# Optimization experiments

Measured on AMD Instinct MI355X. Metric: run time of the kernel, lower is better.

## Reference

```python
import jax, jax.numpy as jnp
import numpy as np

NU, NI, NR = 50000, 50000, 5   # users, items, rating levels
D, B, LS, LI = 64, 512, 32, 64 # embed_dim, batch, max social nbrs, max item hist
NEG = -1e9


def setup_inputs() -> dict:
    key = jax.random.key(0)
    ks = iter(jax.random.split(key, 64))
    def lin(din, dout):
        s = 1.0 / np.sqrt(din)
        return (jax.random.uniform(next(ks), (din, dout), minval=-s, maxval=s, dtype=jnp.float32),
                jax.random.uniform(next(ks), (dout,), minval=-s, maxval=s, dtype=jnp.float32))
    inp = {}
    inp['user_w'] = jax.random.normal(next(ks), (NU, D), dtype=jnp.float32) * 0.1
    inp['item_w'] = jax.random.normal(next(ks), (NI, D), dtype=jnp.float32) * 0.1
    inp['rating_w'] = jax.random.normal(next(ks), (NR, D), dtype=jnp.float32) * 0.1
    for name, din, dout in [('i_ln1', 2*D, D), ('i_ln2', D, D), ('i_ln3', 2*D, D),
                            ('i_att1', 2*D, D), ('i_att2', D, D), ('i_att3', D, 1),
                            ('s_ln1', D, D), ('s_ln2', 2*D, D), ('s_ln3', D, D),
                            ('s_att1', 2*D, D), ('s_att2', D, D), ('s_att3', D, 1)]:
        w, b = lin(din, dout)
        inp[name + '_w'] = w
        inp[name + '_b'] = b
    inp['nodes'] = jax.random.randint(next(ks), (B,), 0, NU)
    inp['social_hist'] = jax.random.randint(next(ks), (NU, LS), 0, NU)
    inp['social_mask'] = jax.random.bernoulli(next(ks), 0.5, (NU, LS)).at[:, 0].set(True)
    inp['item_hist'] = jax.random.randint(next(ks), (NU, LI), 0, NI)
    inp['rating_hist'] = jax.random.randint(next(ks), (NU, LI), 0, NR)
    inp['item_mask'] = jax.random.bernoulli(next(ks), 0.5, (NU, LI)).at[:, 0].set(True)
    return inp


def reference(user_w, item_w, rating_w,
              i_ln1_w, i_ln1_b, i_ln2_w, i_ln2_b, i_ln3_w, i_ln3_b,
              i_att1_w, i_att1_b, i_att2_w, i_att2_b, i_att3_w, i_att3_b,
              s_ln1_w, s_ln1_b, s_ln2_w, s_ln2_b, s_ln3_w, s_ln3_b,
              s_att1_w, s_att1_b, s_att2_w, s_att2_b, s_att3_w, s_att3_b,
              nodes, social_hist, social_mask, item_hist, rating_hist, item_mask):
    relu = jax.nn.relu

    def attn(x, w1, b1, w2, b2, w3, b3, mask):
        # x: [..., L, 2D] -> softmax weights over valid neighbors: [..., L]
        h = relu(x @ w1 + b1)
        h = relu(h @ w2 + b2)
        logit = (h @ w3 + b3)[..., 0]
        logit = jnp.where(mask, logit, NEG)
        return jax.nn.softmax(logit, axis=-1)

    def item_final(uids):
        # uids: any shape [...]; returns [..., D]  (Aggre_item.item_final)
        its, rts, m = item_hist[uids], rating_hist[uids], item_mask[uids]
        x = jnp.concatenate([item_w[its], rating_w[rts]], axis=-1)   # [...,LI,2D]
        x = relu(x @ i_ln1_w + i_ln1_b)                              # [...,LI,D]
        u = user_w[uids]                                             # [...,D]
        a_in = jnp.concatenate([x, jnp.broadcast_to(u[..., None, :], x.shape)], axis=-1)
        alpha = attn(a_in, i_att1_w, i_att1_b, i_att2_w, i_att2_b, i_att3_w, i_att3_b, m)
        hI = jnp.einsum('...l,...ld->...d', alpha, x)                # attention-weighted sum
        hI = relu(hI @ i_ln2_w + i_ln2_b)
        return relu(jnp.concatenate([u, hI], axis=-1) @ i_ln3_w + i_ln3_b)

    # item-space factor of query users
    hI_self = item_final(nodes)                                      # [B,D]
    # social aggregation: item_final over each user's social neighbors
    nbrs, nmask = social_hist[nodes], social_mask[nodes]             # [B,LS]
    hI_nb = item_final(nbrs)                                         # [B,LS,D]
    u = user_w[nodes]                                                # [B,D]
    b_in = jnp.concatenate([hI_nb, jnp.broadcast_to(u[:, None, :], hI_nb.shape)], axis=-1)
    beta = attn(b_in, s_att1_w, s_att1_b, s_att2_w, s_att2_b, s_att3_w, s_att3_b, nmask)
    hS = jnp.einsum('bl,bld->bd', beta, hI_nb)
    hS = relu(hS @ s_ln1_w + s_ln1_b)
    f = jnp.concatenate([hI_self, hS], axis=-1)
    f = relu(f @ s_ln2_w + s_ln2_b)
    return relu(f @ s_ln3_w + s_ln3_b)
```

## Files before the change

### kernel.cpp

```cpp
#include <hip/hip_runtime.h>
#include <math.h>


#define NII 50000
#define BB 512
#define LSS 32
#define NT 16896

typedef short short8 __attribute__((ext_vector_type(8)));
typedef float f32x4 __attribute__((ext_vector_type(4)));

static __device__ __forceinline__ bool mread(const void* p, long i, int mode) {
  if (mode == 0) return ((const int*)p)[i] != 0;
  if (mode == 2) return ((const float*)p)[i] != 0.0f;
  return ((const unsigned char*)p)[i] != 0;
}

static __device__ __forceinline__ float wsum(float v) {
#pragma unroll
  for (int s = 1; s < 64; s <<= 1) v += __shfl_xor(v, s);
  return v;
}
static __device__ __forceinline__ float wmax(float v) {
#pragma unroll
  for (int s = 1; s < 64; s <<= 1) v = fmaxf(v, __shfl_xor(v, s));
  return v;
}
static __device__ __forceinline__ float rsum16(float v) {
#pragma unroll
  for (int s = 1; s < 16; s <<= 1) v += __shfl_xor(v, s);
  return v;
}

static __device__ __forceinline__ short bf16rne(float f) {
  unsigned u = __float_as_uint(f);
  u = (u + 0x7FFFu + ((u >> 16) & 1u)) >> 16;
  return (short)u;
}
static __device__ __forceinline__ float bf16tof(short h) {
  return __uint_as_float(((unsigned)(unsigned short)h) << 16);
}

static __device__ __forceinline__ void wave_fence() {
  asm volatile("s_waitcnt lgkmcnt(0)" ::: "memory");
  __builtin_amdgcn_sched_barrier(0);
}

static __device__ __forceinline__ bool inst_uid(int t, const int* nodes,
                                                const int* social_hist,
                                                const void* social_mask,
                                                int mode, long* uid) {
  if (t < BB) {
    *uid = nodes[t];
    return true;
  }
  const int nb = t - BB;
  const int b = nb >> 5, l = nb & 31;
  const long mi = (long)nodes[b] * LSS + l;
  if (!mread(social_mask, mi, mode)) return false;
  *uid = social_hist[mi];
  return true;
}

__global__ void setup_kernel(const unsigned int* __restrict__ sm,
                             int* __restrict__ flag,
                             const float* __restrict__ rating_w,
                             const float* __restrict__ w1,
                             const float* __restrict__ b1,
                             float* __restrict__ RW1g,
                             const float* __restrict__ A1w,
                             const float* __restrict__ A2w,
                             short* __restrict__ B1,
                             short* __restrict__ B2,
                             short* __restrict__ W1hi,
                             short* __restrict__ W1lo) {
  const int tid = threadIdx.x;
  if (blockIdx.x == 0) {
    __shared__ int notInt, notFloat;
    if (tid == 0) { notInt = 0; notFloat = 0; }
    __syncthreads();
    int ni = 0, nf = 0;
    for (int i = tid; i < 4096; i += 256) {
      unsigned int x = sm[i];
      if (x > 1u) ni = 1;
      if (x != 0u && x != 0x3F800000u) nf = 1;
    }
    if (ni) atomicOr(&notInt, 1);
    if (nf) atomicOr(&notFloat, 1);
    __syncthreads();
    if (tid == 0) flag[0] = notInt ? (notFloat ? 1 : 2) : 0;
  } else if (blockIdx.x == 1) {
    for (int t = tid; t < 320; t += 256) {
      const int r = t >> 6, c = t & 63;
      float acc = b1[c];
      for (int k = 0; k < 64; ++k)
        acc = fmaf(rating_w[r * 64 + k], w1[(64 + k) * 64 + c], acc);
      RW1g[r * 64 + c] = acc;
    }
  } else {
    for (int idx = tid; idx < 4096; idx += 256) {
      int e = idx & 7, g = idx >> 3;
      int l = g & 63, q = g >> 6;
      int kb = q >> 2, nb = q & 3;
      int k = kb * 32 + ((l >> 4) & 3) * 8 + e;
      int col = nb * 16 + (l & 15);
      B1[idx] = bf16rne(A1w[k * 64 + col]);
      B2[idx] = bf16rne(A2w[k * 64 + col]);
      float a = w1[k * 64 + col];
      short h = bf16rne(a);
      W1hi[idx] = h;
      W1lo[idx] = bf16rne(a - bf16tof(h));
    }
  }
}

__global__ __launch_bounds__(256, 2)
void mid_kernel(const float* __restrict__ item_w,
                const short* __restrict__ W1hi,
                const short* __restrict__ W1lo,
                short* __restrict__ xbase16,
                const float* __restrict__ user_w,
                const float* __restrict__ A1w, const float* __restrict__ A1b,
                const int* __restrict__ nodes,
                const int* __restrict__ social_hist,
                float* __restrict__ uA1buf) {
  const int tid = threadIdx.x, lane = tid & 63, w = tid >> 6;
  if (blockIdx.x < 512) {
    const int l15 = lane & 15, lg4 = lane >> 4;
    short8 bh[8], bl[8];
#pragma unroll
    for (int q = 0; q < 8; ++q) {
      bh[q] = *(const short8*)(W1hi + (q * 64 + lane) * 8);
      bl[q] = *(const short8*)(W1lo + (q * 64 + lane) * 8);
    }
    const int wid = blockIdx.x * 4 + w;
    for (int tile = wid; tile < 3125; tile += 2048) {
      const long r0 = (long)tile * 16;
      const float* ap = item_w + (r0 + l15) * 64 + lg4 * 8;
      short8 ah[2], al[2];
#pragma unroll
      for (int kb = 0; kb < 2; ++kb) {
        const float4 a = *(const float4*)(ap + kb * 32);
        const float4 b = *(const float4*)(ap + kb * 32 + 4);
        float v[8] = {a.x, a.y, a.z, a.w, b.x, b.y, b.z, b.w};
        short8 hi, lo;
#pragma unroll
        for (int e = 0; e < 8; ++e) {
          short h = bf16rne(v[e]);
          hi[e] = h;
          lo[e] = bf16rne(v[e] - bf16tof(h));
        }
        ah[kb] = hi;
        al[kb] = lo;
      }
#pragma unroll
      for (int nb = 0; nb < 4; ++nb) {
        f32x4 acc = {0.0f, 0.0f, 0.0f, 0.0f};
        acc = __builtin_amdgcn_mfma_f32_16x16x32_bf16(ah[0], bh[0 * 4 + nb], acc, 0, 0, 0);
        acc = __builtin_amdgcn_mfma_f32_16x16x32_bf16(ah[1], bh[1 * 4 + nb], acc, 0, 0, 0);
        acc = __builtin_amdgcn_mfma_f32_16x16x32_bf16(ah[0], bl[0 * 4 + nb], acc, 0, 0, 0);
        acc = __builtin_amdgcn_mfma_f32_16x16x32_bf16(ah[1], bl[1 * 4 + nb], acc, 0, 0, 0);
        acc = __builtin_amdgcn_mfma_f32_16x16x32_bf16(al[0], bh[0 * 4 + nb], acc, 0, 0, 0);
        acc = __builtin_amdgcn_mfma_f32_16x16x32_bf16(al[1], bh[1 * 4 + nb], acc, 0, 0, 0);
#pragma unroll
        for (int r = 0; r < 4; ++r)
          xbase16[(r0 + lg4 * 4 + r) * 64 + nb * 16 + l15] = bf16rne(acc[r]);
      }
    }
  } else {
    const int i0 = (blockIdx.x - 512) * 64;
    __shared__ float sW[64][64], sU[64][64];
    __shared__ float sb[64];
    __shared__ int sUid[64];
    for (int i = tid; i < 4096; i += 256) sW[i >> 6][i & 63] = A1w[4096 + i];
    if (tid < 64) {
      sb[tid] = A1b[tid];
      const int t = i0 + tid;
      int uid;
      if (t < BB) {
        uid = nodes[t];
      } else {
        const int nb = t - BB;
        uid = social_hist[(long)nodes[nb >> 5] * LSS + (nb & 31)];
      }
      sUid[tid] = uid;
    }
    __syncthreads();
    for (int i = tid; i < 4096; i += 256) {
      int r = i >> 6, c = i & 63;
      sU[r][c] = user_w[(long)sUid[r] * 64 + c];
    }
    __syncthreads();
    float acc[16];
#pragma unroll
    for (int r = 0; r < 16; ++r) acc[r] = sb[lane];
    for (int k = 0; k < 64; k += 4) {
      float wv0 = sW[k][lane], wv1 = sW[k + 1][lane];
      float wv2 = sW[k + 2][lane], wv3 = sW[k + 3][lane];
#pragma unroll
      for (int r = 0; r < 16; ++r) {
        const float4 xv = *(const float4*)(&sU[w * 16 + r][k]);
        acc[r] = fmaf(xv.x, wv0, acc[r]);
        acc[r] = fmaf(xv.y, wv1, acc[r]);
        acc[r] = fmaf(xv.z, wv2, acc[r]);
        acc[r] = fmaf(xv.w, wv3, acc[r]);
      }
    }
#pragma unroll
    for (int r = 0; r < 16; ++r)
      uA1buf[(long)(i0 + w * 16 + r) * 64 + lane] = acc[r];
  }
}

__global__ __launch_bounds__(512, 8)
void core_mfma_kernel(const short* __restrict__ xb16,
                      const float* __restrict__ RW1g,
                      const float* __restrict__ uA1buf,
                      const short* __restrict__ Bimg1,
                      const short* __restrict__ Bimg2,
                      const float* __restrict__ A2b,
                      const float* __restrict__ A3w,
                      const int* __restrict__ item_hist,
                      const int* __restrict__ rating_hist,
                      const void* __restrict__ item_mask,
                      const int* __restrict__ flagp,
                      const int* __restrict__ nodes,
                      const int* __restrict__ social_hist,
                      const void* __restrict__ social_mask,
                      float* __restrict__ hvecbuf) {
  __shared__ __align__(16) short sB1[4096], sB2[4096];
  __shared__ __align__(16) char smem[8][3072];
  const int tid = threadIdx.x, lane = tid & 63, w = tid >> 6;

  short* h1w = (short*)(smem[w]);
  float* lgw = (float*)(smem[w] + 2560);
  int* cw = (int*)(smem[w] + 2816);

  ((int4*)sB1)[tid] = ((const int4*)Bimg1)[tid];
  ((int4*)sB2)[tid] = ((const int4*)Bimg2)[tid];
  __syncthreads();

  const int t = blockIdx.x * 8 + w;
  const int mode = flagp[0];
  long uid;
  if (!inst_uid(t, nodes, social_hist, social_mask, mode, &uid))
    return;

  const float a2bv = A2b[lane];
  const float a3v = A3w[lane];
  const int l15 = lane & 15;
  const int lg4 = lane >> 4;

#define B1F(q) (*(const short8*)(sB1 + ((q) * 64 + lane) * 8))
#define B2F(q) (*(const short8*)(sB2 + ((q) * 64 + lane) * 8))

  const long mbase = uid * 64;
  bool mk = mread(item_mask, mbase + lane, mode);
  unsigned long long bal = __ballot(mk);
  const int nact = (int)__popcll(bal);
  int pos = (int)__popcll(bal & ((1ull << lane) - 1ull));
  if (mk) cw[pos] = (item_hist[mbase + lane] << 3) | rating_hist[mbase + lane];
  const float uA1v = uA1buf[(long)t * 64 + lane];
  wave_fence();

  const int ng = (nact + 15) >> 4;
  for (int mc = 0; mc < ng; ++mc) {
    wave_fence();
    int row = mc * 16 + l15;
    if (row >= nact) row = nact - 1;
    const int p = cw[row];
    const long it = p >> 3;
    const int rt = p & 7;
    short8 xa[2];
#pragma unroll
    for (int kb = 0; kb < 2; ++kb) {
      const int koff = kb * 32 + lg4 * 8;
      const short8 xb = *(const short8*)(xb16 + it * 64 + koff);
      const float* rp = RW1g + rt * 64 + koff;
      const float4 c = *(const float4*)rp;
      const float4 d = *(const float4*)(rp + 4);
      short8 f;
      f[0] = bf16rne(fmaxf(bf16tof(xb[0]) + c.x, 0.0f));
      f[1] = bf16rne(fmaxf(bf16tof(xb[1]) + c.y, 0.0f));
      f[2] = bf16rne(fmaxf(bf16tof(xb[2]) + c.z, 0.0f));
      f[3] = bf16rne(fmaxf(bf16tof(xb[3]) + c.w, 0.0f));
      f[4] = bf16rne(fmaxf(bf16tof(xb[4]) + d.x, 0.0f));
      f[5] = bf16rne(fmaxf(bf16tof(xb[5]) + d.y, 0.0f));
      f[6] = bf16rne(fmaxf(bf16tof(xb[6]) + d.z, 0.0f));
      f[7] = bf16rne(fmaxf(bf16tof(xb[7]) + d.w, 0.0f));
      xa[kb] = f;
    }
#pragma unroll
    for (int nb = 0; nb < 4; ++nb) {
      const float ui = __shfl(uA1v, nb * 16 + l15);
      f32x4 acc = {ui, ui, ui, ui};
      acc = __builtin_amdgcn_mfma_f32_16x16x32_bf16(xa[0], B1F(0 * 4 + nb), acc, 0, 0, 0);
      acc = __builtin_amdgcn_mfma_f32_16x16x32_bf16(xa[1], B1F(1 * 4 + nb), acc, 0, 0, 0);
#pragma unroll
      for (int r = 0; r < 4; ++r)
        h1w[(lg4 * 4 + r) * 80 + nb * 16 + l15] = bf16rne(fmaxf(acc[r], 0.0f));
    }
    wave_fence();
    short8 ha[2];
    ha[0] = *(const short8*)(h1w + l15 * 80 + lg4 * 8);
    ha[1] = *(const short8*)(h1w + l15 * 80 + 32 + lg4 * 8);
    float t0 = 0.0f, t1 = 0.0f, t2 = 0.0f, t3 = 0.0f;
#pragma unroll
    for (int nb = 0; nb < 4; ++nb) {
      const float b2 = __shfl(a2bv, nb * 16 + l15);
      f32x4 acc = {b2, b2, b2, b2};
      acc = __builtin_amdgcn_mfma_f32_16x16x32_bf16(ha[0], B2F(0 * 4 + nb), acc, 0, 0, 0);
      acc = __builtin_amdgcn_mfma_f32_16x16x32_bf16(ha[1], B2F(1 * 4 + nb), acc, 0, 0, 0);
      const float a3c = __shfl(a3v, nb * 16 + l15);
      t0 = fmaf(fmaxf(acc[0], 0.0f), a3c, t0);
      t1 = fmaf(fmaxf(acc[1], 0.0f), a3c, t1);
      t2 = fmaf(fmaxf(acc[2], 0.0f), a3c, t2);
      t3 = fmaf(fmaxf(acc[3], 0.0f), a3c, t3);
    }
    t0 = rsum16(t0); t1 = rsum16(t1); t2 = rsum16(t2); t3 = rsum16(t3);
    if (l15 == 0) {
      const int jb = mc * 16 + lg4 * 4;
      lgw[jb + 0] = t0;
      lgw[jb + 1] = t1;
      lgw[jb + 2] = t2;
      lgw[jb + 3] = t3;
    }
  }
  wave_fence();

  const bool valid = (lane < nact);
  float lv = valid ? lgw[lane] : -1e30f;
  float mx = wmax(lv);
  float e = valid ? __expf(lv - mx) : 0.0f;
  float s = wsum(e);
  const float alpha = e / s;

  float h0 = 0.0f, hA = 0.0f, hB = 0.0f, hC = 0.0f;
  int j = 0;
  for (; j + 3 < nact; j += 4) {
    const int p0 = cw[j], p1 = cw[j + 1], p2 = cw[j + 2], p3 = cw[j + 3];
    const float a0 = __shfl(alpha, j), a1 = __shfl(alpha, j + 1);
    const float a2 = __shfl(alpha, j + 2), a3 = __shfl(alpha, j + 3);
    const float x0 = bf16tof(xb16[(long)(p0 >> 3) * 64 + lane]) + RW1g[(p0 & 7) * 64 + lane];
    const float x1 = bf16tof(xb16[(long)(p1 >> 3) * 64 + lane]) + RW1g[(p1 & 7) * 64 + lane];
    const float x2 = bf16tof(xb16[(long)(p2 >> 3) * 64 + lane]) + RW1g[(p2 & 7) * 64 + lane];
    const float x3 = bf16tof(xb16[(long)(p3 >> 3) * 64 + lane]) + RW1g[(p3 & 7) * 64 + lane];
    h0 = fmaf(a0, fmaxf(x0, 0.0f), h0);
    hA = fmaf(a1, fmaxf(x1, 0.0f), hA);
    hB = fmaf(a2, fmaxf(x2, 0.0f), hB);
    hC = fmaf(a3, fmaxf(x3, 0.0f), hC);
  }
  for (; j < nact; ++j) {
    const int p = cw[j];
    const float aj = __shfl(alpha, j);
    const float xv = bf16tof(xb16[(long)(p >> 3) * 64 + lane]) + RW1g[(p & 7) * 64 + lane];
    h0 = fmaf(aj, fmaxf(xv, 0.0f), h0);
  }
  hvecbuf[(long)t * 64 + lane] = (h0 + hA) + (hB + hC);
#undef B1F
#undef B2F
}

__global__ __launch_bounds__(256, 2)
void hI2final_kernel(const float* __restrict__ hvecbuf,
                     const float* __restrict__ user_w,
                     const float* __restrict__ W2w, const float* __restrict__ W2b,
                     const float* __restrict__ W3w, const float* __restrict__ W3b,
                     const int* __restrict__ nodes,
                     const int* __restrict__ social_hist,
                     float* __restrict__ hIbuf) {
  const int tid = threadIdx.x, lane = tid & 63, w = tid >> 6;
  const int i0 = blockIdx.x * 32;
  __shared__ float sW[128][64];
  __shared__ float sX[32][128];
  __shared__ float sb[64];
  __shared__ int sUid[32];
  for (int i = tid; i < 4096; i += 256) sW[i >> 6][i & 63] = W2w[i];
  if (tid < 64) sb[tid] = W2b[tid];
  if (tid < 32) {
    const int t = i0 + tid;
    int uid;
    if (t < BB) {
      uid = nodes[t];
    } else {
      const int nb = t - BB;
      uid = social_hist[(long)nodes[nb >> 5] * LSS + (nb & 31)];
    }
    sUid[tid] = uid;
  }
  __syncthreads();
  for (int i = tid; i < 2048; i += 256) {
    int r = i >> 6, c = i & 63;
    sX[r][64 + c] = hvecbuf[(long)(i0 + r) * 64 + c];
    sX[r][c] = user_w[(long)sUid[r] * 64 + c];
  }
  __syncthreads();

  float acc[8];
  {
    const float bv = sb[lane];
#pragma unroll
    for (int r = 0; r < 8; ++r) acc[r] = bv;
    for (int k = 0; k < 64; k += 4) {
      float wv0 = sW[k][lane], wv1 = sW[k + 1][lane];
      float wv2 = sW[k + 2][lane], wv3 = sW[k + 3][lane];
#pragma unroll
      for (int r = 0; r < 8; ++r) {
        const float4 xv = *(const float4*)(&sX[w * 8 + r][64 + k]);
        acc[r] = fmaf(xv.x, wv0, acc[r]);
        acc[r] = fmaf(xv.y, wv1, acc[r]);
        acc[r] = fmaf(xv.z, wv2, acc[r]);
        acc[r] = fmaf(xv.w, wv3, acc[r]);
      }
    }
#pragma unroll
    for (int r = 0; r < 8; ++r) sX[w * 8 + r][64 + lane] = fmaxf(acc[r], 0.0f);
  }
  __syncthreads();
  for (int i = tid; i < 8192; i += 256) sW[i >> 6][i & 63] = W3w[i];
  if (tid < 64) sb[tid] = W3b[tid];
  __syncthreads();

  {
    const float bv = sb[lane];
#pragma unroll
    for (int r = 0; r < 8; ++r) acc[r] = bv;
    for (int k = 0; k < 128; k += 4) {
      float wv0 = sW[k][lane], wv1 = sW[k + 1][lane];
      float wv2 = sW[k + 2][lane], wv3 = sW[k + 3][lane];
#pragma unroll
      for (int r = 0; r < 8; ++r) {
        const float4 xv = *(const float4*)(&sX[w * 8 + r][k]);
        acc[r] = fmaf(xv.x, wv0, acc[r]);
        acc[r] = fmaf(xv.y, wv1, acc[r]);
        acc[r] = fmaf(xv.z, wv2, acc[r]);
        acc[r] = fmaf(xv.w, wv3, acc[r]);
      }
    }
#pragma unroll
    for (int r = 0; r < 8; ++r)
      hIbuf[(long)(i0 + w * 8 + r) * 64 + lane] = fmaxf(acc[r], 0.0f);
  }
}

__global__ __launch_bounds__(256, 8)
void social_fused_kernel(const float* __restrict__ hIbuf,
                         const float* __restrict__ user_w,
                         const float* __restrict__ S1w,
                         const float* __restrict__ S1b,
                         const float* __restrict__ S2w,
                         const float* __restrict__ S2b,
                         const float* __restrict__ S3w,
                         const float* __restrict__ L1w, const float* __restrict__ L1b,
                         const float* __restrict__ L2w, const float* __restrict__ L2b,
                         const float* __restrict__ L3w, const float* __restrict__ L3b,
                         const int* __restrict__ nodes,
                         const void* __restrict__ social_mask,
                         const int* __restrict__ flagp,
                         float* __restrict__ out) {
  __shared__ __align__(16) short sB1[4096], sB2[4096];
  __shared__ __align__(16) char smem[4][3584];
  const int tid = threadIdx.x, lane = tid & 63, w = tid >> 6;
  short* h1w = (short*)(smem[w]);
  float* lgw = (float*)(smem[w] + 2560);
  int* cw = (int*)(smem[w] + 2816);
  float* vA = (float*)(smem[w] + 3072);
  float* vB = (float*)(smem[w] + 3328);

  for (int i = tid; i < 4096; i += 256) {
    int e = i & 7, g = i >> 3;
    int l = g & 63, q = g >> 6;
    int kb = q >> 2, nb = q & 3;
    int k = kb * 32 + ((l >> 4) & 3) * 8 + e;
    int col = nb * 16 + (l & 15);
    sB1[i] = bf16rne(S1w[k * 64 + col]);
    sB2[i] = bf16rne(S2w[k * 64 + col]);
  }
  __syncthreads();

  const int mode = flagp[0];
  const int l15 = lane & 15;
  const int lg4 = lane >> 4;
  const int b = blockIdx.x * 4 + w;
  const long uid = nodes[b];

  bool m = (lane < LSS) ? mread(social_mask, uid * LSS + lane, mode) : false;
  unsigned long long bal = __ballot(m);
  const int nval = (int)__popcll(bal);
  int pos = (int)__popcll(bal & ((1ull << lane) - 1ull));
  if (m) cw[pos] = lane;

  const float uv = user_w[uid * 64 + lane];
  float uA1v = S1b[lane];
#pragma unroll 8
  for (int k = 0; k < 64; ++k)
    uA1v = fmaf(__shfl(uv, k), S1w[(64 + k) * 64 + lane], uA1v);
  const float a2bv = S2b[lane];
  const float a3v = S3w[lane];
  wave_fence();

  const long hbase = 512L + (long)b * 32;
  const int ng = (nval + 15) >> 4;
  for (int mc = 0; mc < ng; ++mc) {
    wave_fence();
    int row = mc * 16 + l15;
    if (row >= nval) row = nval - 1;
    const long hrow = hbase + cw[row];
    short8 xa[2];
#pragma unroll
    for (int kb = 0; kb < 2; ++kb) {
      const float* xp = hIbuf + hrow * 64 + kb * 32 + lg4 * 8;
      const float4 a = *(const float4*)xp;
      const float4 bb = *(const float4*)(xp + 4);
      short8 f;
      f[0] = bf16rne(a.x);  f[1] = bf16rne(a.y);
      f[2] = bf16rne(a.z);  f[3] = bf16rne(a.w);
      f[4] = bf16rne(bb.x); f[5] = bf16rne(bb.y);
      f[6] = bf16rne(bb.z); f[7] = bf16rne(bb.w);
      xa[kb] = f;
    }
#pragma unroll
    for (int nb = 0; nb < 4; ++nb) {
      const float ui = __shfl(uA1v, nb * 16 + l15);
      f32x4 acc = {ui, ui, ui, ui};
      acc = __builtin_amdgcn_mfma_f32_16x16x32_bf16(
          xa[0], *(const short8*)(sB1 + ((0 * 4 + nb) * 64 + lane) * 8), acc, 0, 0, 0);
      acc = __builtin_amdgcn_mfma_f32_16x16x32_bf16(
          xa[1], *(const short8*)(sB1 + ((1 * 4 + nb) * 64 + lane) * 8), acc, 0, 0, 0);
#pragma unroll
      for (int r = 0; r < 4; ++r)
        h1w[(lg4 * 4 + r) * 80 + nb * 16 + l15] = bf16rne(fmaxf(acc[r], 0.0f));
    }
    wave_fence();
    short8 ha[2];
    ha[0] = *(const short8*)(h1w + l15 * 80 + lg4 * 8);
    ha[1] = *(const short8*)(h1w + l15 * 80 + 32 + lg4 * 8);
    float t0 = 0.0f, t1 = 0.0f, t2 = 0.0f, t3 = 0.0f;
#pragma unroll
    for (int nb = 0; nb < 4; ++nb) {
      const float b2 = __shfl(a2bv, nb * 16 + l15);
      f32x4 acc = {b2, b2, b2, b2};
      acc = __builtin_amdgcn_mfma_f32_16x16x32_bf16(
          ha[0], *(const short8*)(sB2 + ((0 * 4 + nb) * 64 + lane) * 8), acc, 0, 0, 0);
      acc = __builtin_amdgcn_mfma_f32_16x16x32_bf16(
          ha[1], *(const short8*)(sB2 + ((1 * 4 + nb) * 64 + lane) * 8), acc, 0, 0, 0);
      const float a3c = __shfl(a3v, nb * 16 + l15);
      t0 = fmaf(fmaxf(acc[0], 0.0f), a3c, t0);
      t1 = fmaf(fmaxf(acc[1], 0.0f), a3c, t1);
      t2 = fmaf(fmaxf(acc[2], 0.0f), a3c, t2);
      t3 = fmaf(fmaxf(acc[3], 0.0f), a3c, t3);
    }
    t0 = rsum16(t0); t1 = rsum16(t1); t2 = rsum16(t2); t3 = rsum16(t3);
    if (l15 == 0) {
      const int jb = mc * 16 + lg4 * 4;
      lgw[jb + 0] = t0;
      lgw[jb + 1] = t1;
      lgw[jb + 2] = t2;
      lgw[jb + 3] = t3;
    }
  }
  wave_fence();

  const bool valid = (lane < nval);
  float lv = valid ? lgw[lane] : -1e30f;
  float mx = wmax(lv);
  float e = valid ? __expf(lv - mx) : 0.0f;
  float s = wsum(e);
  const float beta = e / s;

  float hs = 0.0f;
  for (int j = 0; j < nval; ++j) {
    const float bj = __shfl(beta, j);
    hs = fmaf(bj, hIbuf[(hbase + cw[j]) * 64 + lane], hs);
  }

  vA[lane] = hs;
  wave_fence();
  float acc = L1b[lane];
#pragma unroll 8
  for (int k = 0; k < 64; ++k) acc = fmaf(vA[k], L1w[k * 64 + lane], acc);
  const float vecB = fmaxf(acc, 0.0f);
  const float selfv = hIbuf[(long)b * 64 + lane];
  wave_fence();
  vA[lane] = selfv;
  vB[lane] = vecB;
  wave_fence();
  acc = L2b[lane];
#pragma unroll 8
  for (int k = 0; k < 64; ++k) acc = fmaf(vA[k], L2w[k * 64 + lane], acc);
#pragma unroll 8
  for (int k = 0; k < 64; ++k) acc = fmaf(vB[k], L2w[(64 + k) * 64 + lane], acc);
  const float fv = fmaxf(acc, 0.0f);
  wave_fence();
  vA[lane] = fv;
  wave_fence();
  acc = L3b[lane];
#pragma unroll 8
  for (int k = 0; k < 64; ++k) acc = fmaf(vA[k], L3w[k * 64 + lane], acc);
  out[(long)b * 64 + lane] = fmaxf(acc, 0.0f);
}

extern "C" void kernel_launch(void* const* d_in, const int* in_sizes, int n_in,
                              void* d_out, int out_size, void* d_ws, size_t ws_size,
                              hipStream_t stream) {
  const float* user_w   = (const float*)d_in[0];
  const float* item_w   = (const float*)d_in[1];
  const float* rating_w = (const float*)d_in[2];
  const float* i_ln1_w  = (const float*)d_in[3];
  const float* i_ln1_b  = (const float*)d_in[4];
  const float* i_ln2_w  = (const float*)d_in[5];
  const float* i_ln2_b  = (const float*)d_in[6];
  const float* i_ln3_w  = (const float*)d_in[7];
  const float* i_ln3_b  = (const float*)d_in[8];
  const float* i_att1_w = (const float*)d_in[9];
  const float* i_att1_b = (const float*)d_in[10];
  const float* i_att2_w = (const float*)d_in[11];
  const float* i_att2_b = (const float*)d_in[12];
  const float* i_att3_w = (const float*)d_in[13];
  const float* i_att3_b = (const float*)d_in[14];
  const float* s_ln1_w  = (const float*)d_in[15];
  const float* s_ln1_b  = (const float*)d_in[16];
  const float* s_ln2_w  = (const float*)d_in[17];
  const float* s_ln2_b  = (const float*)d_in[18];
  const float* s_ln3_w  = (const float*)d_in[19];
  const float* s_ln3_b  = (const float*)d_in[20];
  const float* s_att1_w = (const float*)d_in[21];
  const float* s_att1_b = (const float*)d_in[22];
  const float* s_att2_w = (const float*)d_in[23];
  const float* s_att2_b = (const float*)d_in[24];
  const float* s_att3_w = (const float*)d_in[25];
  const float* s_att3_b = (const float*)d_in[26];
  const int*  nodes       = (const int*)d_in[27];
  const int*  social_hist = (const int*)d_in[28];
  const void* social_mask = d_in[29];
  const int*  item_hist   = (const int*)d_in[30];
  const int*  rating_hist = (const int*)d_in[31];
  const void* item_mask   = d_in[32];

  char* ws = (char*)d_ws;
  int*   flag    = (int*)(ws + 0);
  float* uA1buf  = (float*)(ws + 135680);
  float* hIbuf   = uA1buf;
  float* hvecbuf = (float*)(ws + 4461056);
  short* W1hi    = (short*)(ws + 4461056);
  short* W1lo    = (short*)(ws + 4469248);
  short* xbase16 = (short*)(ws + 8786432);
  float* RW1g    = (float*)(ws + 21586432);
  short* Bimg1   = (short*)(ws + 21587712);
  short* Bimg2   = (short*)(ws + 21595904);

  setup_kernel<<<3, 256, 0, stream>>>(
      (const unsigned int*)social_mask, flag,
      rating_w, i_ln1_w, i_ln1_b, RW1g,
      i_att1_w, i_att2_w, Bimg1, Bimg2, W1hi, W1lo);
  mid_kernel<<<512 + NT / 64, 256, 0, stream>>>(
      item_w, W1hi, W1lo, xbase16,
      user_w, i_att1_w, i_att1_b, nodes, social_hist, uA1buf);
  core_mfma_kernel<<<NT / 8, 512, 0, stream>>>(
      xbase16, RW1g, uA1buf, Bimg1, Bimg2, i_att2_b, i_att3_w,
      item_hist, rating_hist, item_mask, flag,
      nodes, social_hist, social_mask, hvecbuf);
  hI2final_kernel<<<NT / 32, 256, 0, stream>>>(
      hvecbuf, user_w, i_ln2_w, i_ln2_b, i_ln3_w, i_ln3_b,
      nodes, social_hist, hIbuf);
  social_fused_kernel<<<BB / 4, 256, 0, stream>>>(
      hIbuf, user_w, s_att1_w, s_att1_b, s_att2_w, s_att2_b, s_att3_w,
      s_ln1_w, s_ln1_b, s_ln2_w, s_ln2_b, s_ln3_w, s_ln3_b,
      nodes, social_mask, flag, (float*)d_out);
}
```

Measured before the change: 107.8 us.

## Fuse online softmax and weighted sum into MFMA attention loop, reusing gathered rows

Replaces the separate logit-store, full-wave softmax and second gather pass over item embeddings with an online (running max/sum) softmax computed per 16-row chunk. The weighted sum is accumulated from the bf16 A-fragments already loaded for the MFMA, which avoids re-reading xb16 and RW1 from global memory. It adds 16 per-lane accumulators and extra cross-lane reductions, and the weighted sum now uses bf16-rounded inputs instead of fp32-added values, which slightly changes numerics. The h1 LDS row pitch is also changed from 80 to 72 shorts.

```diff
diff --git a/kernel.cpp b/kernel.cpp
--- a/kernel.cpp
+++ b/kernel.cpp
@@ -29,6 +29,11 @@
 static __device__ __forceinline__ float rsum16(float v) {
 #pragma unroll
   for (int s = 1; s < 16; s <<= 1) v += __shfl_xor(v, s);
+  return v;
+}
+static __device__ __forceinline__ float rmax16(float v) {
+#pragma unroll
+  for (int s = 1; s < 16; s <<= 1) v = fmaxf(v, __shfl_xor(v, s));
   return v;
 }
 
@@ -233,8 +238,8 @@
   const int tid = threadIdx.x, lane = tid & 63, w = tid >> 6;
 
   short* h1w = (short*)(smem[w]);
-  float* lgw = (float*)(smem[w] + 2560);
   int* cw = (int*)(smem[w] + 2816);
+  float* vAw = (float*)(smem[w]);
 
   ((int4*)sB1)[tid] = ((const int4*)Bimg1)[tid];
   ((int4*)sB2)[tid] = ((const int4*)Bimg2)[tid];
@@ -263,10 +268,16 @@
   const float uA1v = uA1buf[(long)t * 64 + lane];
   wave_fence();
 
+  float m = -1e30f, s = 0.0f;
+  float hIa[16];
+#pragma unroll
+  for (int q = 0; q < 16; ++q) hIa[q] = 0.0f;
+
   const int ng = (nact + 15) >> 4;
   for (int mc = 0; mc < ng; ++mc) {
     wave_fence();
     int row = mc * 16 + l15;
+    const bool vld = (row < nact);
     if (row >= nact) row = nact - 1;
     const int p = cw[row];
     const long it = p >> 3;
@@ -298,12 +309,12 @@
       acc = __builtin_amdgcn_mfma_f32_16x16x32_bf16(xa[1], B1F(1 * 4 + nb), acc, 0, 0, 0);
 #pragma unroll
       for (int r = 0; r < 4; ++r)
-        h1w[(lg4 * 4 + r) * 80 + nb * 16 + l15] = bf16rne(fmaxf(acc[r], 0.0f));
+        h1w[(lg4 * 4 + r) * 72 + nb * 16 + l15] = bf16rne(fmaxf(acc[r], 0.0f));
     }
     wave_fence();
     short8 ha[2];
-    ha[0] = *(const short8*)(h1w + l15 * 80 + lg4 * 8);
-    ha[1] = *(const short8*)(h1w + l15 * 80 + 32 + lg4 * 8);
+    ha[0] = *(const short8*)(h1w + l15 * 72 + lg4 * 8);
+    ha[1] = *(const short8*)(h1w + l15 * 72 + 32 + lg4 * 8);
     float t0 = 0.0f, t1 = 0.0f, t2 = 0.0f, t3 = 0.0f;
 #pragma unroll
     for (int nb = 0; nb < 4; ++nb) {
@@ -318,45 +329,37 @@
       t3 = fmaf(fmaxf(acc[3], 0.0f), a3c, t3);
     }
     t0 = rsum16(t0); t1 = rsum16(t1); t2 = rsum16(t2); t3 = rsum16(t3);
-    if (l15 == 0) {
-      const int jb = mc * 16 + lg4 * 4;
-      lgw[jb + 0] = t0;
-      lgw[jb + 1] = t1;
-      lgw[jb + 2] = t2;
-      lgw[jb + 3] = t3;
-    }
-  }
-  wave_fence();
-
-  const bool valid = (lane < nact);
-  float lv = valid ? lgw[lane] : -1e30f;
-  float mx = wmax(lv);
-  float e = valid ? __expf(lv - mx) : 0.0f;
-  float s = wsum(e);
-  const float alpha = e / s;
-
-  float h0 = 0.0f, hA = 0.0f, hB = 0.0f, hC = 0.0f;
-  int j = 0;
-  for (; j + 3 < nact; j += 4) {
-    const int p0 = cw[j], p1 = cw[j + 1], p2 = cw[j + 2], p3 = cw[j + 3];
-    const float a0 = __shfl(alpha, j), a1 = __shfl(alpha, j + 1);
-    const float a2 = __shfl(alpha, j + 2), a3 = __shfl(alpha, j + 3);
-    const float x0 = bf16tof(xb16[(long)(p0 >> 3) * 64 + lane]) + RW1g[(p0 & 7) * 64 + lane];
-    const float x1 = bf16tof(xb16[(long)(p1 >> 3) * 64 + lane]) + RW1g[(p1 & 7) * 64 + lane];
-    const float x2 = bf16tof(xb16[(long)(p2 >> 3) * 64 + lane]) + RW1g[(p2 & 7) * 64 + lane];
-    const float x3 = bf16tof(xb16[(long)(p3 >> 3) * 64 + lane]) + RW1g[(p3 & 7) * 64 + lane];
-    h0 = fmaf(a0, fmaxf(x0, 0.0f), h0);
-    hA = fmaf(a1, fmaxf(x1, 0.0f), hA);
-    hB = fmaf(a2, fmaxf(x2, 0.0f), hB);
-    hC = fmaf(a3, fmaxf(x3, 0.0f), hC);
-  }
-  for (; j < nact; ++j) {
-    const int p = cw[j];
-    const float aj = __shfl(alpha, j);
-    const float xv = bf16tof(xb16[(long)(p >> 3) * 64 + lane]) + RW1g[(p & 7) * 64 + lane];
-    h0 = fmaf(aj, fmaxf(xv, 0.0f), h0);
-  }
-  hvecbuf[(long)t * 64 + lane] = (h0 + hA) + (hB + hC);
+    const int srcl = ((l15 >> 2) << 4) | l15;
+    const float v0 = __shfl(t0, srcl), v1 = __shfl(t1, srcl);
+    const float v2 = __shfl(t2, srcl), v3 = __shfl(t3, srcl);
+    float lv = (l15 & 2) ? ((l15 & 1) ? v3 : v2) : ((l15 & 1) ? v1 : v0);
+    lv = vld ? lv : -1e30f;
+    const float cm = rmax16(lv);
+    const float mn = fmaxf(m, cm);
+    const float scale = __expf(m - mn);
+    const float e = vld ? __expf(lv - mn) : 0.0f;
+    s = s * scale + rsum16(e);
+    m = mn;
+#pragma unroll
+    for (int q = 0; q < 8; ++q) {
+      hIa[q] = fmaf(hIa[q], scale, e * bf16tof(xa[0][q]));
+      hIa[8 + q] = fmaf(hIa[8 + q], scale, e * bf16tof(xa[1][q]));
+    }
+  }
+  wave_fence();
+
+  const float inv = 1.0f / s;
+#pragma unroll
+  for (int q = 0; q < 16; ++q) hIa[q] = rsum16(hIa[q] * inv);
+  if (l15 == 0) {
+#pragma unroll
+    for (int e = 0; e < 8; ++e) {
+      vAw[lg4 * 8 + e] = hIa[e];
+      vAw[32 + lg4 * 8 + e] = hIa[8 + e];
+    }
+  }
+  wave_fence();
+  hvecbuf[(long)t * 64 + lane] = vAw[lane];
 #undef B1F
 #undef B2F
 }
```

Measured after the change: 119.2 us. +10.6%, slower.
